# Optimization experiments

Hardware: AMD Instinct MI355X
Metric: run time of the kernel (lower is better)

## Reference

```python
import jax, jax.numpy as jnp
import numpy as np

N = 50000
E = 800000
F_IN = 128
HID = 32
NEG_SLOPE = 0.2  # PyG GATConv default


def _gat_layer(x, src, dst, W, a_src, a_dst, b, heads, out_c, concat, n_nodes):
    # Linear transform per head: [N, heads, out_c]
    h = (x @ W).reshape(n_nodes, heads, out_c)
    # Per-node attention logits per head
    al_src = jnp.einsum('nhc,hc->nh', h, a_src)  # source contribution
    al_dst = jnp.einsum('nhc,hc->nh', h, a_dst)  # destination contribution
    # Edge logits (message j=src -> i=dst), leaky relu
    e = jax.nn.leaky_relu(al_src[src] + al_dst[dst], NEG_SLOPE)  # [E', heads]
    # Segment softmax over incoming edges of each destination node
    m = jax.ops.segment_max(e, dst, num_segments=n_nodes)
    ex = jnp.exp(e - m[dst])
    denom = jax.ops.segment_sum(ex, dst, num_segments=n_nodes)
    alpha = ex / denom[dst]  # [E', heads]; self-loops guarantee denom > 0
    # Weighted scatter-aggregate of source features
    msg = h[src] * alpha[:, :, None]  # [E', heads, out_c]
    out = jax.ops.segment_sum(msg, dst, num_segments=n_nodes)  # [N, heads, out_c]
    out = out.reshape(n_nodes, heads * out_c) if concat else out.mean(axis=1)
    return out + b


def setup_inputs() -> dict:
    key = jax.random.key(0)
    ks = jax.random.split(key, 10)
    x = jax.random.normal(ks[0], (N, F_IN), dtype=jnp.float32)
    edge_index = jax.random.randint(ks[1], (2, E), 0, N, dtype=jnp.int64)
    s = 0.1
    return {
        'x': x,
        'edge_index': edge_index,
        'W1': jax.random.normal(ks[2], (F_IN, 4 * HID), dtype=jnp.float32) * s,
        'a_src1': jax.random.normal(ks[3], (4, HID), dtype=jnp.float32) * s,
        'a_dst1': jax.random.normal(ks[4], (4, HID), dtype=jnp.float32) * s,
        'b1': jnp.zeros((4 * HID,), jnp.float32),
        'W2': jax.random.normal(ks[5], (4 * HID, 2 * HID), dtype=jnp.float32) * s,
        'a_src2': jax.random.normal(ks[6], (2, HID), dtype=jnp.float32) * s,
        'a_dst2': jax.random.normal(ks[7], (2, HID), dtype=jnp.float32) * s,
        'b2': jnp.zeros((2 * HID,), jnp.float32),
        'W3': jax.random.normal(ks[8], (2 * HID, 1), dtype=jnp.float32) * s,
        'a_src3': jax.random.normal(ks[9], (1, 1), dtype=jnp.float32) * s,
        'a_dst3': jax.random.normal(jax.random.fold_in(key, 99), (1, 1), dtype=jnp.float32) * s,
        'b3': jnp.zeros((1,), jnp.float32),
    }


def reference(x, edge_index, W1, a_src1, a_dst1, b1, W2, a_src2, a_dst2, b2, W3, a_src3, a_dst3, b3):
    n = x.shape[0]
    # add_self_loops=True (PyG default)
    loop = jnp.arange(n, dtype=edge_index.dtype)
    src = jnp.concatenate([edge_index[0], loop])
    dst = jnp.concatenate([edge_index[1], loop])
    h = _gat_layer(x, src, dst, W1, a_src1, a_dst1, b1, 4, HID, True, n)
    h = jax.nn.elu(h)  # dropout is identity in eval mode
    h = _gat_layer(h, src, dst, W2, a_src2, a_dst2, b2, 2, HID, True, n)
    h = jax.nn.elu(h)
    out = _gat_layer(h, src, dst, W3, a_src3, a_dst3, b3, 1, 1, False, n)
    return out  # [N, 1]
```

## Files before the change

kernel.cpp:

```cpp
#include <hip/hip_runtime.h>
#include <hip/hip_fp16.h>
#include <math.h>

#define F_IN 128
constexpr int SB = 256;

__global__ void count_deg4(const int* __restrict__ dst, int* __restrict__ deg, int E) {
    int t = blockIdx.x * 256 + threadIdx.x;
    int base = t * 4;
    if (base + 3 < E) {
        int4 d = *(const int4*)(dst + base);
        atomicAdd(&deg[d.x], 1);
        atomicAdd(&deg[d.y], 1);
        atomicAdd(&deg[d.z], 1);
        atomicAdd(&deg[d.w], 1);
    } else {
        for (int k = 0; k < 4; ++k) {
            int e = base + k;
            if (e < E) atomicAdd(&deg[dst[e]], 1);
        }
    }
}

__global__ void scan1(const int* __restrict__ in, int* __restrict__ out,
                      int* __restrict__ bsums, int n, int selfN) {
    __shared__ int sm[SB];
    int i = blockIdx.x * SB + threadIdx.x;
    int v = (i < n) ? (in[i] + (i < selfN ? 1 : 0)) : 0;
    sm[threadIdx.x] = v;
    __syncthreads();
    for (int d = 1; d < SB; d <<= 1) {
        int t = (threadIdx.x >= d) ? sm[threadIdx.x - d] : 0;
        __syncthreads();
        sm[threadIdx.x] += t;
        __syncthreads();
    }
    if (i < n) out[i] = sm[threadIdx.x] - v;
    if (threadIdx.x == SB - 1) bsums[blockIdx.x] = sm[SB - 1];
}

__global__ void scan2(int* __restrict__ bsums, int nb) {
    __shared__ int sm[SB];
    int v = (threadIdx.x < nb) ? bsums[threadIdx.x] : 0;
    sm[threadIdx.x] = v;
    __syncthreads();
    for (int d = 1; d < SB; d <<= 1) {
        int t = (threadIdx.x >= d) ? sm[threadIdx.x - d] : 0;
        __syncthreads();
        sm[threadIdx.x] += t;
        __syncthreads();
    }
    if (threadIdx.x < nb) bsums[threadIdx.x] = sm[threadIdx.x] - v;
}

__global__ void scan3(int* __restrict__ off, int* __restrict__ cursor,
                      const int* __restrict__ bsums, int n, int ncur) {
    int i = blockIdx.x * SB + threadIdx.x;
    if (i < n) {
        int v = off[i] + bsums[blockIdx.x];
        off[i] = v;
        if (i < ncur) cursor[i] = v;
    }
}

template <int BN, int TN, int HEADS, typename AT>
__device__ __forceinline__ void gemm_dev(
    const AT* __restrict__ A, const float* __restrict__ B,
    const float* __restrict__ asrc, const float* __restrict__ adst,
    __half* __restrict__ C, float* __restrict__ als, float* __restrict__ ald,
    int M, int bid) {
    constexpr int BM = 128, BK = 16, TM = 4, K = 128;
    __shared__ float As[BK][BM + 4];
    __shared__ float Bs[BK][BN];
    const int tx = threadIdx.x, ty = threadIdx.y;
    const int tid = ty * 16 + tx;
    const int row0 = bid * BM;
    const int i0 = ty * TM;
    const int j0a = tx * 4;
    const int j0b = 64 + tx * 4;

    float acc[TM][TN];
#pragma unroll
    for (int m = 0; m < TM; ++m)
#pragma unroll
        for (int n = 0; n < TN; ++n) acc[m][n] = 0.f;

    const int ar = tid >> 2;
    const int ak = (tid & 3) * 4;
    int arow = row0 + ar;
    if (arow >= M) arow = M - 1;
    const AT* Aptr = A + (size_t)arow * K + ak;
    const int bk = (BN == 128) ? (tid >> 5) : (tid >> 4);
    const int bc = (BN == 128) ? ((tid & 31) * 4) : ((tid & 15) * 4);
    const bool bact = (BN == 128) || (tid < 256);

    for (int kc = 0; kc < K; kc += BK) {
        float a0, a1v, a2v, a3v;
        if constexpr (sizeof(AT) == 4) {
            float4 av = *(const float4*)(Aptr + kc);
            a0 = av.x; a1v = av.y; a2v = av.z; a3v = av.w;
        } else {
            uint2 raw = *(const uint2*)(Aptr + kc);
            __half2 h01 = *(__half2*)&raw.x;
            __half2 h23 = *(__half2*)&raw.y;
            float2 f01 = __half22float2(h01);
            float2 f23 = __half22float2(h23);
            a0 = f01.x; a1v = f01.y; a2v = f23.x; a3v = f23.y;
        }
        float4 bv;
        if (bact) bv = *(const float4*)(B + (size_t)(kc + bk) * BN + bc);
        __syncthreads();
        As[ak + 0][ar] = a0;
        As[ak + 1][ar] = a1v;
        As[ak + 2][ar] = a2v;
        As[ak + 3][ar] = a3v;
        if (bact) *(float4*)&Bs[bk][bc] = bv;
        __syncthreads();
#pragma unroll
        for (int kk = 0; kk < BK; ++kk) {
            float4 a4 = *(const float4*)&As[kk][i0];
            float arr[TM] = {a4.x, a4.y, a4.z, a4.w};
            float br[TN];
            float4 b0 = *(const float4*)&Bs[kk][j0a];
            br[0] = b0.x; br[1] = b0.y; br[2] = b0.z; br[3] = b0.w;
            if constexpr (TN == 8) {
                float4 b1 = *(const float4*)&Bs[kk][j0b];
                br[4] = b1.x; br[5] = b1.y; br[6] = b1.z; br[7] = b1.w;
            }
#pragma unroll
            for (int m = 0; m < TM; ++m)
#pragma unroll
                for (int n = 0; n < TN; ++n) acc[m][n] += arr[m] * br[n];
        }
    }

#pragma unroll
    for (int m = 0; m < TM; ++m) {
        int row = row0 + i0 + m;
        bool ok = row < M;
        if constexpr (TN == 8) {
            if (ok) {
                alignas(8) __half2 pa[2], pb[2];
#pragma unroll
                for (int n2 = 0; n2 < 2; ++n2) {
                    pa[n2] = __floats2half2_rn(acc[m][2 * n2], acc[m][2 * n2 + 1]);
                    pb[n2] = __floats2half2_rn(acc[m][4 + 2 * n2], acc[m][5 + 2 * n2]);
                }
                *(uint2*)&C[(size_t)row * BN + j0a] = *(uint2*)pa;
                *(uint2*)&C[(size_t)row * BN + j0b] = *(uint2*)pb;
            }
            float psA = 0.f, pdA = 0.f, psB = 0.f, pdB = 0.f;
#pragma unroll
            for (int n = 0; n < 4; ++n) {
                psA += acc[m][n] * asrc[j0a + n];
                pdA += acc[m][n] * adst[j0a + n];
                psB += acc[m][n + 4] * asrc[j0b + n];
                pdB += acc[m][n + 4] * adst[j0b + n];
            }
#pragma unroll
            for (int msk = 1; msk < 8; msk <<= 1) {
                psA += __shfl_xor(psA, msk, 64);
                pdA += __shfl_xor(pdA, msk, 64);
                psB += __shfl_xor(psB, msk, 64);
                pdB += __shfl_xor(pdB, msk, 64);
            }
            if (ok && (tx & 7) == 0) {
                int hA = tx >> 3;
                als[row * HEADS + hA] = psA;
                ald[row * HEADS + hA] = pdA;
                als[row * HEADS + 2 + hA] = psB;
                ald[row * HEADS + 2 + hA] = pdB;
            }
        } else {
            if (ok) {
                alignas(8) __half2 ph[2];
#pragma unroll
                for (int n2 = 0; n2 < 2; ++n2)
                    ph[n2] = __floats2half2_rn(acc[m][2 * n2], acc[m][2 * n2 + 1]);
                *(uint2*)&C[(size_t)row * BN + j0a] = *(uint2*)ph;
            }
            float ps = 0.f, pd = 0.f;
#pragma unroll
            for (int n = 0; n < TN; ++n) {
                ps += acc[m][n] * asrc[j0a + n];
                pd += acc[m][n] * adst[j0a + n];
            }
#pragma unroll
            for (int msk = 1; msk < 8; msk <<= 1) {
                ps += __shfl_xor(ps, msk, 64);
                pd += __shfl_xor(pd, msk, 64);
            }
            if (ok && (tx & 7) == 0) {
                int h0 = tx >> 3;
                als[row * HEADS + h0] = ps;
                ald[row * HEADS + h0] = pd;
            }
        }
    }
}

__global__ __launch_bounds__(512) void gemm1_scatter(
    const float* __restrict__ A, const float* __restrict__ B,
    const float* __restrict__ asrc, const float* __restrict__ adst,
    __half* __restrict__ C, float* __restrict__ als, float* __restrict__ ald,
    int M, int gblk,
    const int* __restrict__ src, const int* __restrict__ dst,
    int* __restrict__ cursor, int* __restrict__ csr, int E, int N) {
    if ((int)blockIdx.x < gblk) {
        gemm_dev<128, 8, 4, float>(A, B, asrc, adst, C, als, ald, M, blockIdx.x);
        return;
    }
    int tid = threadIdx.y * 16 + threadIdx.x;
    int g = blockIdx.x & 7;
    int c = (blockIdx.x - gblk) >> 3;
    int t = c * 512 + tid;
    int E4 = (E + 3) >> 2;
    int nspan = (N + 7) >> 3;
    int r0 = g * nspan;
    int r1 = r0 + nspan; if (r1 > N) r1 = N;
    if (t < E4) {
        int base = t * 4;
        if (base + 3 < E) {
            int4 s4 = *(const int4*)(src + base);
            int4 d4 = *(const int4*)(dst + base);
            if (d4.x >= r0 && d4.x < r1) { int p = atomicAdd(&cursor[d4.x], 1); csr[p] = s4.x; }
            if (d4.y >= r0 && d4.y < r1) { int p = atomicAdd(&cursor[d4.y], 1); csr[p] = s4.y; }
            if (d4.z >= r0 && d4.z < r1) { int p = atomicAdd(&cursor[d4.z], 1); csr[p] = s4.z; }
            if (d4.w >= r0 && d4.w < r1) { int p = atomicAdd(&cursor[d4.w], 1); csr[p] = s4.w; }
        } else {
            for (int k = 0; k < 4; ++k) {
                int e = base + k;
                if (e < E) {
                    int d = dst[e];
                    if (d >= r0 && d < r1) {
                        int p = atomicAdd(&cursor[d], 1);
                        csr[p] = src[e];
                    }
                }
            }
        }
    } else {
        int i = t - E4;
        if (i >= r0 && i < r1) {
            int p = atomicAdd(&cursor[i], 1);
            csr[p] = i;
        }
    }
}

template <int BN, int TN, int HEADS>
__global__ __launch_bounds__(512) void gemm_fused_h(
    const __half* __restrict__ A, const float* __restrict__ B,
    const float* __restrict__ asrc, const float* __restrict__ adst,
    __half* __restrict__ C, float* __restrict__ als, float* __restrict__ ald,
    int M) {
    gemm_dev<BN, TN, HEADS, __half>(A, B, asrc, adst, C, als, ald, M, blockIdx.x);
}

__global__ void gat_agg_l1(const __half* __restrict__ h,
                           const float* __restrict__ als, const float* __restrict__ ald,
                           const float* __restrict__ bias,
                           const int* __restrict__ off, const int* __restrict__ csr,
                           __half* __restrict__ out, int n) {
    constexpr int P = 8;
    int wid = (blockIdx.x * blockDim.x + threadIdx.x) >> 6;
    int lane = threadIdx.x & 63;
    if (wid >= n) return;
    const int hd = lane >> 4;
    const __half2* h2 = (const __half2*)h + lane;
    float ad = ald[wid * 4 + hd];
    int e0 = off[wid], e1 = off[wid + 1];
    float Sx = 0.f, Sy = 0.f, D = 0.f;

    float al[P];
    __half2 hv[P];
#pragma unroll
    for (int p = 0; p < P; ++p) {
        int ee = e0 + p;
        int ie = (ee < e1) ? ee : e1 - 1;
        int s = csr[ie];
        float av = als[s * 4 + hd];
        al[p] = (ee < e1) ? av : -1e30f;
        hv[p] = h2[(size_t)s * 64];
    }
    int e = e0;
    for (; e + P < e1; e += P) {
        float nal[P];
        __half2 nhv[P];
#pragma unroll
        for (int p = 0; p < P; ++p) {
            int ee = e + P + p;
            int ie = (ee < e1) ? ee : e1 - 1;
            int s = csr[ie];
            float av = als[s * 4 + hd];
            nal[p] = (ee < e1) ? av : -1e30f;
            nhv[p] = h2[(size_t)s * 64];
        }
#pragma unroll
        for (int p = 0; p < P; ++p) {
            float lg = al[p] + ad;
            lg = lg > 0.f ? lg : 0.2f * lg;
            float exv = __expf(lg);
            D += exv;
            Sx = fmaf(exv, __low2float(hv[p]), Sx);
            Sy = fmaf(exv, __high2float(hv[p]), Sy);
            al[p] = nal[p];
            hv[p] = nhv[p];
        }
    }
#pragma unroll
    for (int p = 0; p < P; ++p) {
        float lg = al[p] + ad;
        lg = lg > 0.f ? lg : 0.2f * lg;
        float exv = __expf(lg);
        D += exv;
        Sx = fmaf(exv, __low2float(hv[p]), Sx);
        Sy = fmaf(exv, __high2float(hv[p]), Sy);
    }

    float inv = 1.f / D;
    float2 bv = ((const float2*)bias)[lane];
    float vx = Sx * inv + bv.x, vy = Sy * inv + bv.y;
    vx = vx > 0.f ? vx : (__expf(vx) - 1.f);
    vy = vy > 0.f ? vy : (__expf(vy) - 1.f);
    ((__half2*)out)[(size_t)wid * 64 + lane] = __floats2half2_rn(vx, vy);
}

__global__ void gat_agg_l2(const __half* __restrict__ h,
                           const float* __restrict__ als, const float* __restrict__ ald,
                           const float* __restrict__ bias,
                           const int* __restrict__ off, const int* __restrict__ csr,
                           const float* __restrict__ W3, const float* __restrict__ as3,
                           const float* __restrict__ ad3, float2* __restrict__ hs,
                           float* __restrict__ ald3, int n) {
    constexpr int P = 8;
    int wid = (blockIdx.x * blockDim.x + threadIdx.x) >> 6;
    int lane = threadIdx.x & 63;
    if (wid >= n) return;
    const int hd = lane >> 5;
    const __half* hp = h + lane;
    float ad = ald[wid * 2 + hd];
    int e0 = off[wid], e1 = off[wid + 1];
    float S = 0.f, D = 0.f;

    float al[P];
    __half hv[P];
#pragma unroll
    for (int p = 0; p < P; ++p) {
        int ee = e0 + p;
        int ie = (ee < e1) ? ee : e1 - 1;
        int s = csr[ie];
        float av = als[s * 2 + hd];
        al[p] = (ee < e1) ? av : -1e30f;
        hv[p] = hp[(size_t)s * 64];
    }
    int e = e0;
    for (; e + P < e1; e += P) {
        float nal[P];
        __half nhv[P];
#pragma unroll
        for (int p = 0; p < P; ++p) {
            int ee = e + P + p;
            int ie = (ee < e1) ? ee : e1 - 1;
            int s = csr[ie];
            float av = als[s * 2 + hd];
            nal[p] = (ee < e1) ? av : -1e30f;
            nhv[p] = hp[(size_t)s * 64];
        }
#pragma unroll
        for (int p = 0; p < P; ++p) {
            float lg = al[p] + ad;
            lg = lg > 0.f ? lg : 0.2f * lg;
            float exv = __expf(lg);
            D += exv;
            S = fmaf(exv, __half2float(hv[p]), S);
            al[p] = nal[p];
            hv[p] = nhv[p];
        }
    }
#pragma unroll
    for (int p = 0; p < P; ++p) {
        float lg = al[p] + ad;
        lg = lg > 0.f ? lg : 0.2f * lg;
        float exv = __expf(lg);
        D += exv;
        S = fmaf(exv, __half2float(hv[p]), S);
    }

    float v = S / D + bias[lane];
    v = v > 0.f ? v : (__expf(v) - 1.f);
    float r = v * W3[lane];
#pragma unroll
    for (int msk = 1; msk < 64; msk <<= 1) r += __shfl_xor(r, msk, 64);
    if (lane == 0) {
        hs[wid] = make_float2(r, r * as3[0]);
        ald3[wid] = r * ad3[0];
    }
}

__global__ void gat_agg1(const float2* __restrict__ hs, const float* __restrict__ ald3,
                         const float* __restrict__ bias,
                         const int* __restrict__ off, const int* __restrict__ csr,
                         float* __restrict__ out, int n) {
    int i = blockIdx.x * blockDim.x + threadIdx.x;
    if (i >= n) return;
    float ad = ald3[i];
    int e0 = off[i], e1 = off[i + 1];
    float S = 0.f, D = 0.f;
    float2 g[2];
    float valid[2];
#pragma unroll
    for (int p = 0; p < 2; ++p) {
        int ee = e0 + p;
        int ie = (ee < e1) ? ee : e1 - 1;
        int s = csr[ie];
        g[p] = hs[s];
        valid[p] = (ee < e1) ? 0.f : -1e30f;
    }
    int e = e0;
    for (; e + 2 < e1; e += 2) {
#pragma unroll
        for (int p = 0; p < 2; ++p) {
            int ee = e + 2 + p;
            int ie = (ee < e1) ? ee : e1 - 1;
            int s = csr[ie];
            float2 ng = hs[s];
            float nvalid = (ee < e1) ? 0.f : -1e30f;
            float lg = g[p].y + ad + valid[p];
            lg = lg > 0.f ? lg : 0.2f * lg;
            float exv = __expf(lg);
            D += exv;
            S = fmaf(exv, g[p].x, S);
            g[p] = ng;
            valid[p] = nvalid;
        }
    }
#pragma unroll
    for (int p = 0; p < 2; ++p) {
        float lg = g[p].y + ad + valid[p];
        lg = lg > 0.f ? lg : 0.2f * lg;
        float exv = __expf(lg);
        D += exv;
        S = fmaf(exv, g[p].x, S);
    }
    out[i] = S / D + bias[0];
}

extern "C" void kernel_launch(void* const* d_in, const int* in_sizes, int n_in,
                              void* d_out, int out_size, void* d_ws, size_t ws_size,
                              hipStream_t stream) {
    const float* x   = (const float*)d_in[0];
    const int*   ei  = (const int*)d_in[1];
    const float* W1  = (const float*)d_in[2];
    const float* as1 = (const float*)d_in[3];
    const float* ad1 = (const float*)d_in[4];
    const float* b1  = (const float*)d_in[5];
    const float* W2  = (const float*)d_in[6];
    const float* as2 = (const float*)d_in[7];
    const float* ad2 = (const float*)d_in[8];
    const float* b2  = (const float*)d_in[9];
    const float* W3  = (const float*)d_in[10];
    const float* as3 = (const float*)d_in[11];
    const float* ad3 = (const float*)d_in[12];
    const float* b3  = (const float*)d_in[13];
    float* out = (float*)d_out;

    const int N = in_sizes[0] / F_IN;
    const int E = in_sizes[1] / 2;
    const int ET = E + N;

    char* w = (char*)d_ws;
    size_t o = 0;
    auto alloc = [&](size_t bytes) -> void* {
        void* p = w + o;
        o += (bytes + 255) & ~(size_t)255;
        return p;
    };
    __half* hbuf = (__half*)alloc((size_t)N * 128 * 2);
    __half* a1   = (__half*)alloc((size_t)N * 128 * 2);
    float2* hs   = (float2*)alloc((size_t)N * 8);
    float* als  = (float*)alloc((size_t)N * 4 * 4);
    float* ald  = (float*)alloc((size_t)N * 4 * 4);
    float* ald3 = (float*)alloc((size_t)N * 4);
    int* deg    = (int*)alloc((size_t)(N + 1) * 4);
    int* off    = (int*)alloc((size_t)(N + 1) * 4);
    int* cursor = (int*)alloc((size_t)N * 4);
    int* bsums  = (int*)alloc(1024);
    int* csr    = (int*)alloc((size_t)ET * 4);

    __half* h2 = hbuf;

    const int* esrc = ei;
    const int* edst = ei + E;

    hipMemsetAsync(deg, 0, (size_t)(N + 1) * 4, stream);
    count_deg4<<<((E + 3) / 4 + 255) / 256, 256, 0, stream>>>(edst, deg, E);
    int n1 = N + 1;
    int nb = (n1 + SB - 1) / SB;
    scan1<<<nb, SB, 0, stream>>>(deg, off, bsums, n1, N);
    scan2<<<1, SB, 0, stream>>>(bsums, nb);
    scan3<<<nb, SB, 0, stream>>>(off, cursor, bsums, n1, N);

    const int gblk = (N + 127) / 128;

    {
        int E4 = (E + 3) >> 2;
        int spg = (E4 + N + 511) / 512;
        int sblk = 8 * spg;
        gemm1_scatter<<<gblk + sblk, dim3(16, 32), 0, stream>>>(
            x, W1, as1, ad1, hbuf, als, ald, N, gblk,
            esrc, edst, cursor, csr, E, N);
    }

    gat_agg_l1<<<(N * 64 + 255) / 256, 256, 0, stream>>>(
        hbuf, als, ald, b1, off, csr, a1, N);

    gemm_fused_h<64, 4, 2><<<gblk, dim3(16, 32), 0, stream>>>(
        a1, W2, as2, ad2, h2, als, ald, N);
    gat_agg_l2<<<(N * 64 + 255) / 256, 256, 0, stream>>>(
        h2, als, ald, b2, off, csr, W3, as3, ad3, hs, ald3, N);

    gat_agg1<<<(N + 255) / 256, 256, 0, stream>>>(hs, ald3, b3, off, csr, out, N);
}
```

Baseline: 205.5 us.

## Vectorize GAT aggregation gathers with 16-byte loads across edge subgroups

The layer-1 and layer-2 aggregation kernels now split each wavefront into lane groups that process different edges in parallel. Each lane gathers 8 halves with a single 16-byte load instead of one half or half2 per lane, and partial sums are combined across groups with shuffles. The attention logits are pre-scaled by log2(e) in the GEMM epilogue so the softmax can use exp2f, with leaky ReLU written as fmaxf. The aim is fewer, wider gather instructions and more edges in flight per wavefront, at the cost of extra cross-lane reductions and masked padding lanes on low-degree nodes.

```diff
diff --git a/kernel.cpp b/kernel.cpp
--- a/kernel.cpp
+++ b/kernel.cpp
@@ -4,6 +4,7 @@
 
 #define F_IN 128
 constexpr int SB = 256;
+constexpr float LOG2E = 1.4426950408889634f;
 
 __global__ void count_deg4(const int* __restrict__ dst, int* __restrict__ deg, int E) {
     int t = blockIdx.x * 256 + threadIdx.x;
@@ -166,10 +167,10 @@
             }
             if (ok && (tx & 7) == 0) {
                 int hA = tx >> 3;
-                als[row * HEADS + hA] = psA;
-                ald[row * HEADS + hA] = pdA;
-                als[row * HEADS + 2 + hA] = psB;
-                ald[row * HEADS + 2 + hA] = pdB;
+                als[row * HEADS + hA] = psA * LOG2E;
+                ald[row * HEADS + hA] = pdA * LOG2E;
+                als[row * HEADS + 2 + hA] = psB * LOG2E;
+                ald[row * HEADS + 2 + hA] = pdB * LOG2E;
             }
         } else {
             if (ok) {
@@ -192,8 +193,8 @@
             }
             if (ok && (tx & 7) == 0) {
                 int h0 = tx >> 3;
-                als[row * HEADS + h0] = ps;
-                ald[row * HEADS + h0] = pd;
+                als[row * HEADS + h0] = ps * LOG2E;
+                ald[row * HEADS + h0] = pd * LOG2E;
             }
         }
     }
@@ -262,68 +263,81 @@
                            const float* __restrict__ bias,
                            const int* __restrict__ off, const int* __restrict__ csr,
                            __half* __restrict__ out, int n) {
-    constexpr int P = 8;
     int wid = (blockIdx.x * blockDim.x + threadIdx.x) >> 6;
     int lane = threadIdx.x & 63;
     if (wid >= n) return;
-    const int hd = lane >> 4;
-    const __half2* h2 = (const __half2*)h + lane;
+    const int g = lane >> 4;
+    const int q = lane & 15;
+    const int hd = q >> 2;
     float ad = ald[wid * 4 + hd];
     int e0 = off[wid], e1 = off[wid + 1];
-    float Sx = 0.f, Sy = 0.f, D = 0.f;
-
-    float al[P];
-    __half2 hv[P];
-#pragma unroll
-    for (int p = 0; p < P; ++p) {
-        int ee = e0 + p;
+    const __half* hq = h + q * 8;
+
+    float acc[8] = {0.f, 0.f, 0.f, 0.f, 0.f, 0.f, 0.f, 0.f};
+    float D = 0.f;
+
+    auto LD = [&](int ebase, uint4& h4, float& al) {
+        int ee = ebase + g;
         int ie = (ee < e1) ? ee : e1 - 1;
         int s = csr[ie];
         float av = als[s * 4 + hd];
-        al[p] = (ee < e1) ? av : -1e30f;
-        hv[p] = h2[(size_t)s * 64];
-    }
+        al = (ee < e1) ? av : -1e30f;
+        h4 = *(const uint4*)(hq + (size_t)s * 128);
+    };
+    auto PROC = [&](const uint4& h4, float al) {
+        float lg = al + ad;
+        lg = fmaxf(lg, 0.2f * lg);
+        float exv = exp2f(lg);
+        D += exv;
+        const __half2* hh = (const __half2*)&h4;
+#pragma unroll
+        for (int i = 0; i < 4; ++i) {
+            float2 f = __half22float2(hh[i]);
+            acc[2 * i] = fmaf(exv, f.x, acc[2 * i]);
+            acc[2 * i + 1] = fmaf(exv, f.y, acc[2 * i + 1]);
+        }
+    };
+
+    uint4 hA, hB;
+    float alA, alB;
+    LD(e0, hA, alA);
+    LD(e0 + 4, hB, alB);
     int e = e0;
-    for (; e + P < e1; e += P) {
-        float nal[P];
-        __half2 nhv[P];
-#pragma unroll
-        for (int p = 0; p < P; ++p) {
-            int ee = e + P + p;
-            int ie = (ee < e1) ? ee : e1 - 1;
-            int s = csr[ie];
-            float av = als[s * 4 + hd];
-            nal[p] = (ee < e1) ? av : -1e30f;
-            nhv[p] = h2[(size_t)s * 64];
-        }
-#pragma unroll
-        for (int p = 0; p < P; ++p) {
-            float lg = al[p] + ad;
-            lg = lg > 0.f ? lg : 0.2f * lg;
-            float exv = __expf(lg);
-            D += exv;
-            Sx = fmaf(exv, __low2float(hv[p]), Sx);
-            Sy = fmaf(exv, __high2float(hv[p]), Sy);
-            al[p] = nal[p];
-            hv[p] = nhv[p];
-        }
-    }
-#pragma unroll
-    for (int p = 0; p < P; ++p) {
-        float lg = al[p] + ad;
-        lg = lg > 0.f ? lg : 0.2f * lg;
-        float exv = __expf(lg);
-        D += exv;
-        Sx = fmaf(exv, __low2float(hv[p]), Sx);
-        Sy = fmaf(exv, __high2float(hv[p]), Sy);
-    }
-
-    float inv = 1.f / D;
-    float2 bv = ((const float2*)bias)[lane];
-    float vx = Sx * inv + bv.x, vy = Sy * inv + bv.y;
-    vx = vx > 0.f ? vx : (__expf(vx) - 1.f);
-    vy = vy > 0.f ? vy : (__expf(vy) - 1.f);
-    ((__half2*)out)[(size_t)wid * 64 + lane] = __floats2half2_rn(vx, vy);
+    for (; e + 8 < e1; e += 8) {
+        uint4 nA, nB;
+        float nalA, nalB;
+        LD(e + 8, nA, nalA);
+        LD(e + 12, nB, nalB);
+        PROC(hA, alA);
+        PROC(hB, alB);
+        hA = nA; alA = nalA;
+        hB = nB; alB = nalB;
+    }
+    PROC(hA, alA);
+    PROC(hB, alB);
+
+#pragma unroll
+    for (int i = 0; i < 8; ++i) {
+        acc[i] += __shfl_xor(acc[i], 16, 64);
+        acc[i] += __shfl_xor(acc[i], 32, 64);
+    }
+    D += __shfl_xor(D, 16, 64);
+    D += __shfl_xor(D, 32, 64);
+
+    if (g == 0) {
+        float inv = 1.f / D;
+        alignas(16) __half2 ph[4];
+#pragma unroll
+        for (int i = 0; i < 4; ++i) {
+            float2 bv = ((const float2*)bias)[q * 4 + i];
+            float vx = acc[2 * i] * inv + bv.x;
+            float vy = acc[2 * i + 1] * inv + bv.y;
+            vx = vx > 0.f ? vx : (__expf(vx) - 1.f);
+            vy = vy > 0.f ? vy : (__expf(vy) - 1.f);
+            ph[i] = __floats2half2_rn(vx, vy);
+        }
+        *(uint4*)(out + (size_t)wid * 128 + q * 8) = *(uint4*)ph;
+    }
 }
 
 __global__ void gat_agg_l2(const __half* __restrict__ h,
@@ -333,68 +347,82 @@
                            const float* __restrict__ W3, const float* __restrict__ as3,
                            const float* __restrict__ ad3, float2* __restrict__ hs,
                            float* __restrict__ ald3, int n) {
-    constexpr int P = 8;
     int wid = (blockIdx.x * blockDim.x + threadIdx.x) >> 6;
     int lane = threadIdx.x & 63;
     if (wid >= n) return;
-    const int hd = lane >> 5;
-    const __half* hp = h + lane;
+    const int g = lane >> 3;
+    const int q = lane & 7;
+    const int hd = q >> 2;
     float ad = ald[wid * 2 + hd];
     int e0 = off[wid], e1 = off[wid + 1];
-    float S = 0.f, D = 0.f;
-
-    float al[P];
-    __half hv[P];
-#pragma unroll
-    for (int p = 0; p < P; ++p) {
-        int ee = e0 + p;
+    const __half* hq = h + q * 8;
+
+    float acc[8] = {0.f, 0.f, 0.f, 0.f, 0.f, 0.f, 0.f, 0.f};
+    float D = 0.f;
+
+    auto LD = [&](int ebase, uint4& h4, float& al) {
+        int ee = ebase + g;
         int ie = (ee < e1) ? ee : e1 - 1;
         int s = csr[ie];
         float av = als[s * 2 + hd];
-        al[p] = (ee < e1) ? av : -1e30f;
-        hv[p] = hp[(size_t)s * 64];
-    }
+        al = (ee < e1) ? av : -1e30f;
+        h4 = *(const uint4*)(hq + (size_t)s * 64);
+    };
+    auto PROC = [&](const uint4& h4, float al) {
+        float lg = al + ad;
+        lg = fmaxf(lg, 0.2f * lg);
+        float exv = exp2f(lg);
+        D += exv;
+        const __half2* hh = (const __half2*)&h4;
+#pragma unroll
+        for (int i = 0; i < 4; ++i) {
+            float2 f = __half22float2(hh[i]);
+            acc[2 * i] = fmaf(exv, f.x, acc[2 * i]);
+            acc[2 * i + 1] = fmaf(exv, f.y, acc[2 * i + 1]);
+        }
+    };
+
+    uint4 hA, hB;
+    float alA, alB;
+    LD(e0, hA, alA);
+    LD(e0 + 8, hB, alB);
     int e = e0;
-    for (; e + P < e1; e += P) {
-        float nal[P];
-        __half nhv[P];
-#pragma unroll
-        for (int p = 0; p < P; ++p) {
-            int ee = e + P + p;
-            int ie = (ee < e1) ? ee : e1 - 1;
-            int s = csr[ie];
-            float av = als[s * 2 + hd];
-            nal[p] = (ee < e1) ? av : -1e30f;
-            nhv[p] = hp[(size_t)s * 64];
-        }
-#pragma unroll
-        for (int p = 0; p < P; ++p) {
-            float lg = al[p] + ad;
-            lg = lg > 0.f ? lg : 0.2f * lg;
-            float exv = __expf(lg);
-            D += exv;
-            S = fmaf(exv, __half2float(hv[p]), S);
-            al[p] = nal[p];
-            hv[p] = nhv[p];
-        }
-    }
-#pragma unroll
-    for (int p = 0; p < P; ++p) {
-        float lg = al[p] + ad;
-        lg = lg > 0.f ? lg : 0.2f * lg;
-        float exv = __expf(lg);
-        D += exv;
-        S = fmaf(exv, __half2float(hv[p]), S);
-    }
-
-    float v = S / D + bias[lane];
-    v = v > 0.f ? v : (__expf(v) - 1.f);
-    float r = v * W3[lane];
-#pragma unroll
-    for (int msk = 1; msk < 64; msk <<= 1) r += __shfl_xor(r, msk, 64);
+    for (; e + 16 < e1; e += 16) {
+        uint4 nA, nB;
+        float nalA, nalB;
+        LD(e + 16, nA, nalA);
+        LD(e + 24, nB, nalB);
+        PROC(hA, alA);
+        PROC(hB, alB);
+        hA = nA; alA = nalA;
+        hB = nB; alB = nalB;
+    }
+    PROC(hA, alA);
+    PROC(hB, alB);
+
+#pragma unroll
+    for (int i = 0; i < 8; ++i) {
+        acc[i] += __shfl_xor(acc[i], 8, 64);
+        acc[i] += __shfl_xor(acc[i], 16, 64);
+        acc[i] += __shfl_xor(acc[i], 32, 64);
+    }
+    D += __shfl_xor(D, 8, 64);
+    D += __shfl_xor(D, 16, 64);
+    D += __shfl_xor(D, 32, 64);
+
+    float inv = 1.f / D;
+    float r = 0.f;
+#pragma unroll
+    for (int i = 0; i < 8; ++i) {
+        float v = acc[i] * inv + bias[q * 8 + i];
+        v = v > 0.f ? v : (__expf(v) - 1.f);
+        r = fmaf(v, W3[q * 8 + i], r);
+    }
+#pragma unroll
+    for (int msk = 1; msk < 8; msk <<= 1) r += __shfl_xor(r, msk, 64);
     if (lane == 0) {
-        hs[wid] = make_float2(r, r * as3[0]);
-        ald3[wid] = r * ad3[0];
+        hs[wid] = make_float2(r, r * as3[0] * LOG2E);
+        ald3[wid] = r * ad3[0] * LOG2E;
     }
 }
 
@@ -427,8 +455,8 @@
             float2 ng = hs[s];
             float nvalid = (ee < e1) ? 0.f : -1e30f;
             float lg = g[p].y + ad + valid[p];
-            lg = lg > 0.f ? lg : 0.2f * lg;
-            float exv = __expf(lg);
+            lg = fmaxf(lg, 0.2f * lg);
+            float exv = exp2f(lg);
             D += exv;
             S = fmaf(exv, g[p].x, S);
             g[p] = ng;
@@ -438,8 +466,8 @@
 #pragma unroll
     for (int p = 0; p < 2; ++p) {
         float lg = g[p].y + ad + valid[p];
-        lg = lg > 0.f ? lg : 0.2f * lg;
-        float exv = __expf(lg);
+        lg = fmaxf(lg, 0.2f * lg);
+        float exv = exp2f(lg);
         D += exv;
         S = fmaf(exv, g[p].x, S);
     }
```

Result: faster. 182.2 us (-11.3%).
